# Kernel tuning notes

Hardware: AMD Instinct MI355X
Metric: run time of the kernel (lower is better)

Reference implementation:

```python
import jax, jax.numpy as jnp
import numpy as np

B, S, D = 16, 2048, 2048  # S == D required for m_q + output broadcast in original code


def setup_inputs() -> dict:
    key = jax.random.key(0)
    ks = jax.random.split(key, 8)
    scale = 1.0 / np.sqrt(D)
    return {
        "hidden_list": jax.random.normal(ks[0], (B, S, D), dtype=jnp.float32),
        "m_q": jax.random.normal(ks[1], (D,), dtype=jnp.float32),
        "Wq": jax.random.normal(ks[2], (D, D), dtype=jnp.float32) * scale,
        "bq": jax.random.normal(ks[3], (D,), dtype=jnp.float32) * scale,
        "Wm": jax.random.normal(ks[4], (D, D), dtype=jnp.float32) * scale,
        "bm": jax.random.normal(ks[5], (D,), dtype=jnp.float32) * scale,
        "Wa": jax.random.normal(ks[6], (D, D), dtype=jnp.float32) * scale,
        "ba": jax.random.normal(ks[7], (D,), dtype=jnp.float32) * scale,
    }


def reference(hidden_list, m_q, Wq, bq, Wm, bm, Wa, ba):
    # hidden_list: [B, S, D]; m_q: [D]
    hq = jnp.tanh(jnp.einsum("bsd,ed->bse", hidden_list, Wq) + bq)      # [B,S,D]
    mq = jnp.tanh(Wm @ m_q + bm)                                        # [D]
    Sg = hq * mq                                                        # gated bilinear, [B,S,D]
    alpha = jax.nn.softmax(jnp.einsum("bsd,ed->bse", Sg, Wa) + ba, axis=-1)  # [B,S,D]
    output = jnp.sum(alpha * hidden_list, axis=-1)                      # [B,S]
    m_q_new = m_q + output                                              # broadcast [D]+[B,S] (S==D)
    return output, m_q_new
```

## Files before the change

### kernel.cpp

```cpp
#include <hip/hip_runtime.h>

typedef unsigned short u16;
typedef short bf16x8 __attribute__((ext_vector_type(8)));
typedef u16 u16x8 __attribute__((ext_vector_type(8)));
typedef float f32x4 __attribute__((ext_vector_type(4)));

__device__ __forceinline__ float bf2f(u16 u) {
    union { unsigned u; float f; } c; c.u = ((unsigned)u) << 16; return c.f;
}
__device__ __forceinline__ u16 f2bf(float f) {
    union { float f; unsigned u; } c; c.f = f;
    unsigned r = c.u + 0x7FFFu + ((c.u >> 16) & 1u);
    return (u16)(r >> 16);
}
__device__ __forceinline__ float tanh_fast(float x) {
    float e = __expf(2.0f * x);
    return 1.0f - 2.0f / (e + 1.0f);
}
__device__ __forceinline__ void gll16(const void* g, void* l) {
    __builtin_amdgcn_global_load_lds((const __attribute__((address_space(1))) void*)g,
                                     (__attribute__((address_space(3))) void*)l, 16, 0, 0);
}

#define BAR() do { __builtin_amdgcn_sched_barrier(0); __builtin_amdgcn_s_barrier(); \
                   __builtin_amdgcn_sched_barrier(0); } while (0)

__global__ __launch_bounds__(256) void cvt_f32_bf16(const float* __restrict__ src,
                                                    u16* __restrict__ dst, int n8) {
    int i = blockIdx.x * blockDim.x + threadIdx.x;
    int stride = gridDim.x * blockDim.x;
    for (; i < n8; i += stride) {
        const float4* s = (const float4*)(src + (size_t)i * 8);
        float4 a = s[0], b = s[1];
        u16x8 o;
        o[0] = f2bf(a.x); o[1] = f2bf(a.y); o[2] = f2bf(a.z); o[3] = f2bf(a.w);
        o[4] = f2bf(b.x); o[5] = f2bf(b.y); o[6] = f2bf(b.z); o[7] = f2bf(b.w);
        *(u16x8*)(dst + (size_t)i * 8) = o;
    }
}

__global__ __launch_bounds__(256) void mq_kernel(const float* __restrict__ Wm,
                                                 const float* __restrict__ q,
                                                 const float* __restrict__ bm,
                                                 float* __restrict__ mq, int D) {
    int w = threadIdx.x >> 6, l = threadIdx.x & 63;
    int e = blockIdx.x * 4 + w;
    const float* wp = Wm + (size_t)e * D;
    float s = 0.f;
    for (int j = 0; j < D; j += 256) {
        float4 wv = *(const float4*)(wp + j + l * 4);
        float4 qv = *(const float4*)(q + j + l * 4);
        s += wv.x * qv.x + wv.y * qv.y + wv.z * qv.z + wv.w * qv.w;
    }
    #pragma unroll
    for (int o = 32; o >= 1; o >>= 1) s += __shfl_xor(s, o);
    if (l == 0) mq[e] = tanh_fast(s + bm[e]);
}

template <int EPI>
__global__ __launch_bounds__(512, 2) void gemm8(const u16* __restrict__ A,
                                                const u16* __restrict__ B,
                                                const float* __restrict__ bias,
                                                const float* __restrict__ gate,
                                                u16* __restrict__ C,
                                                int M, int N, int K) {
    __shared__ u16 sh[65536];
    char* LDS = (char*)sh;
    const int K2 = K * 2;
    const int KT = K >> 6;

    const int tid = threadIdx.x;
    const int w = tid >> 6, l = tid & 63;
    const int wm = w >> 2, wn = w & 3;

    int orig = blockIdx.x + gridDim.x * blockIdx.y;
    int nwg = gridDim.x * gridDim.y;
    int id = ((nwg & 7) == 0) ? ((orig & 7) * (nwg >> 3) + (orig >> 3)) : orig;
    const int tileN = (id % gridDim.x) * 256;
    const int tileM = (id / gridDim.x) * 256;

    const int r0 = (w * 2) * 8 + (l >> 3);
    const int r1 = (w * 2 + 1) * 8 + (l >> 3);
    const int cc = ((l & 7) ^ (l >> 3)) << 4;
    const char* srcA0 = (const char*)A + (size_t)(tileM + r0) * K2 + cc;
    const char* srcA1 = (const char*)A + (size_t)(tileM + r1) * K2 + cc;
    const char* srcB0 = (const char*)B + (size_t)(tileN + r0) * K2 + cc;
    const char* srcB1 = (const char*)B + (size_t)(tileN + r1) * K2 + cc;
    const int ldc0 = (w * 2) * 1024, ldc1 = (w * 2 + 1) * 1024;

#define STG_A(tk, h) do { size_t go = (size_t)(tk) * 128 + (size_t)(h) * 128 * K2; \
    int sb = ((((tk) & 1) * 2 + (h)) * 16384); \
    gll16(srcA0 + go, LDS + sb + ldc0); gll16(srcA1 + go, LDS + sb + ldc1); } while (0)
#define STG_B(tk, h) do { size_t go = (size_t)(tk) * 128 + (size_t)(h) * 128 * K2; \
    int sb = 65536 + ((((tk) & 1) * 2 + (h)) * 16384); \
    gll16(srcB0 + go, LDS + sb + ldc0); gll16(srcB1 + go, LDS + sb + ldc1); } while (0)

    const int sw = l & 7;
    const int rowA = (wm * 64 + (l & 15)) * 128;
    const int rowB = (wn * 32 + (l & 15)) * 128;
    const int ck0 = (((l >> 4) ^ sw) << 4);
    const int ck1 = (((4 + (l >> 4)) ^ sw) << 4);
    const char* pA0 = LDS + rowA + ck0;
    const char* pA1 = LDS + rowA + ck1;
    const char* pB0 = LDS + 65536 + rowB + ck0;
    const char* pB1 = LDS + 65536 + rowB + ck1;

    f32x4 acc[2][4][2][2] = {};

    STG_A(0, 0); STG_A(0, 1); STG_B(0, 0); STG_B(0, 1);
    STG_A(1, 0); STG_B(1, 0);
    asm volatile("s_waitcnt vmcnt(4)" ::: "memory");
    BAR();

#define MFMA_CLUSTER(QM, QN, AF, BF)                                            \
    __builtin_amdgcn_s_setprio(1);                                              \
    _Pragma("unroll")                                                           \
    for (int fm = 0; fm < 4; ++fm)                                              \
        _Pragma("unroll")                                                       \
        for (int fn = 0; fn < 2; ++fn) {                                        \
            acc[QM][fm][QN][fn] = __builtin_amdgcn_mfma_f32_16x16x32_bf16(      \
                AF[fm][0], BF[fn][0], acc[QM][fm][QN][fn], 0, 0, 0);            \
            acc[QM][fm][QN][fn] = __builtin_amdgcn_mfma_f32_16x16x32_bf16(      \
                AF[fm][1], BF[fn][1], acc[QM][fm][QN][fn], 0, 0, 0);            \
        }                                                                       \
    __builtin_amdgcn_s_setprio(0);

#define ITER(t, P) do {                                                         \
    constexpr int A0O = (2 * (P)) * 16384;                                      \
    constexpr int A1O = (2 * (P) + 1) * 16384;                                  \
    bf16x8 af[4][2], b0[2][2], b1[2][2];                                        \
                                   \
    _Pragma("unroll")                                                           \
    for (int fm = 0; fm < 4; ++fm) {                                            \
        af[fm][0] = *(const bf16x8*)(pA0 + A0O + fm * 2048);                    \
        af[fm][1] = *(const bf16x8*)(pA1 + A0O + fm * 2048);                    \
    }                                                                           \
    _Pragma("unroll")                                                           \
    for (int fn = 0; fn < 2; ++fn) {                                            \
        b0[fn][0] = *(const bf16x8*)(pB0 + A0O + fn * 2048);                    \
        b0[fn][1] = *(const bf16x8*)(pB1 + A0O + fn * 2048);                    \
    }                                                                           \
    if ((t) + 1 < KT) STG_A((t) + 1, 1);                                        \
    BAR();                                                                      \
    MFMA_CLUSTER(0, 0, af, b0)                                                  \
    BAR();                                                                      \
                                       \
    _Pragma("unroll")                                                           \
    for (int fn = 0; fn < 2; ++fn) {                                            \
        b1[fn][0] = *(const bf16x8*)(pB0 + A1O + fn * 2048);                    \
        b1[fn][1] = *(const bf16x8*)(pB1 + A1O + fn * 2048);                    \
    }                                                                           \
    if ((t) + 1 < KT) STG_B((t) + 1, 1);                                        \
    BAR();                                                                      \
    MFMA_CLUSTER(0, 1, af, b1)                                                  \
    BAR();                                                                      \
                                       \
    _Pragma("unroll")                                                           \
    for (int fm = 0; fm < 4; ++fm) {                                            \
        af[fm][0] = *(const bf16x8*)(pA0 + A1O + fm * 2048);                    \
        af[fm][1] = *(const bf16x8*)(pA1 + A1O + fm * 2048);                    \
    }                                                                           \
    if ((t) + 2 < KT) STG_A((t) + 2, 0);                                        \
    BAR();                                                                      \
    MFMA_CLUSTER(1, 0, af, b0)                                                  \
    BAR();                                                                      \
                                     \
    if ((t) + 2 < KT) STG_B((t) + 2, 0);                                        \
    BAR();                                                                      \
    MFMA_CLUSTER(1, 1, af, b1)                                                  \
    if ((t) + 2 < KT) asm volatile("s_waitcnt vmcnt(4)" ::: "memory");          \
    else              asm volatile("s_waitcnt vmcnt(0)" ::: "memory");          \
    BAR();                                                                      \
} while (0)

    for (int tt = 0; tt < KT; tt += 2) {
        ITER(tt, 0);
        ITER(tt + 1, 1);
    }
#undef ITER
#undef MFMA_CLUSTER
#undef STG_A
#undef STG_B

    const int cr = (l >> 4) * 4;
    const int cl = l & 15;
    #pragma unroll
    for (int qn = 0; qn < 2; ++qn)
        #pragma unroll
        for (int fn = 0; fn < 2; ++fn) {
            const int col = tileN + qn * 128 + wn * 32 + fn * 16 + cl;
            const float bs = bias[col];
            float gt = 0.f;
            if (EPI == 0) gt = gate[col];
            #pragma unroll
            for (int qm = 0; qm < 2; ++qm)
                #pragma unroll
                for (int fm = 0; fm < 4; ++fm)
                    #pragma unroll
                    for (int r = 0; r < 4; ++r) {
                        const int row = tileM + qm * 128 + wm * 64 + fm * 16 + cr + r;
                        float v = acc[qm][fm][qn][fn][r] + bs;
                        if (EPI == 0) v = tanh_fast(v) * gt;
                        C[(size_t)row * N + col] = f2bf(v);
                    }
        }
}

__global__ __launch_bounds__(256) void softmax_out(const u16* __restrict__ logits,
                                                   const float* __restrict__ hidden,
                                                   const float* __restrict__ m_q,
                                                   float* __restrict__ out,
                                                   int D, int R) {
    const int r = blockIdx.x;
    const int t = threadIdx.x;
    const int w = t >> 6, l = t & 63;
    const u16* lp = logits + (size_t)r * D + t * 8;
    const float* hp = hidden + (size_t)r * D + t * 8;

    bf16x8 lv = *(const bf16x8*)lp;
    float lf[8];
    #pragma unroll
    for (int j = 0; j < 8; ++j) lf[j] = bf2f((u16)lv[j]);
    float4 h0 = *(const float4*)hp;
    float4 h1 = *(const float4*)(hp + 4);
    float hv[8] = {h0.x, h0.y, h0.z, h0.w, h1.x, h1.y, h1.z, h1.w};

    float m = lf[0];
    #pragma unroll
    for (int j = 1; j < 8; ++j) m = fmaxf(m, lf[j]);
    #pragma unroll
    for (int o = 32; o >= 1; o >>= 1) m = fmaxf(m, __shfl_xor(m, o));

    __shared__ float red[8];
    if (l == 0) red[w] = m;
    __syncthreads();
    m = fmaxf(fmaxf(red[0], red[1]), fmaxf(red[2], red[3]));
    __syncthreads();

    float se = 0.f, sh = 0.f;
    #pragma unroll
    for (int j = 0; j < 8; ++j) {
        float e = __expf(lf[j] - m);
        se += e;
        sh += e * hv[j];
    }
    #pragma unroll
    for (int o = 32; o >= 1; o >>= 1) { se += __shfl_xor(se, o); sh += __shfl_xor(sh, o); }
    if (l == 0) { red[w] = se; red[4 + w] = sh; }
    __syncthreads();
    if (t == 0) {
        float SE = red[0] + red[1] + red[2] + red[3];
        float SH = red[4] + red[5] + red[6] + red[7];
        float o = SH / SE;
        out[r] = o;
        out[R + r] = m_q[r & (D - 1)] + o;
    }
}

extern "C" void kernel_launch(void* const* d_in, const int* in_sizes, int n_in,
                              void* d_out, int out_size, void* d_ws, size_t ws_size,
                              hipStream_t stream) {
    const float* hidden = (const float*)d_in[0];
    const float* m_q    = (const float*)d_in[1];
    const float* Wq     = (const float*)d_in[2];
    const float* bq     = (const float*)d_in[3];
    const float* Wm     = (const float*)d_in[4];
    const float* bm     = (const float*)d_in[5];
    const float* Wa     = (const float*)d_in[6];
    const float* ba     = (const float*)d_in[7];
    float* out = (float*)d_out;

    const int D = 2048;
    const int M = 16 * 2048;

    char* ws = (char*)d_ws;
    size_t oH  = 0;
    size_t oS  = oH  + (size_t)M * D * 2;
    size_t oWq = oS  + (size_t)M * D * 2;
    size_t oWa = oWq + (size_t)D * D * 2;
    size_t oMq = oWa + (size_t)D * D * 2;
    size_t need = oMq + (size_t)D * sizeof(float);
    if (ws_size < need) return;

    u16* hbf    = (u16*)(ws + oH);
    u16* Sg     = (u16*)(ws + oS);
    u16* Wqb    = (u16*)(ws + oWq);
    u16* Wab    = (u16*)(ws + oWa);
    float* mq   = (float*)(ws + oMq);
    u16* logits = hbf;

    cvt_f32_bf16<<<4096, 256, 0, stream>>>(hidden, hbf, M * D / 8);
    cvt_f32_bf16<<<1024, 256, 0, stream>>>(Wq, Wqb, D * D / 8);
    cvt_f32_bf16<<<1024, 256, 0, stream>>>(Wa, Wab, D * D / 8);
    mq_kernel<<<D / 4, 256, 0, stream>>>(Wm, m_q, bm, mq, D);

    dim3 grid(D / 256, M / 256);
    gemm8<0><<<grid, 512, 0, stream>>>(hbf, Wqb, bq, mq, Sg, M, D, D);
    gemm8<1><<<grid, 512, 0, stream>>>(Sg, Wab, ba, nullptr, logits, M, D, D);

    softmax_out<<<M, 256, 0, stream>>>(logits, hidden, m_q, out, D, M);
}
```

Baseline: 659.7 us.

## Software-pipeline LDS fragment loads with MFMA clusters and cut barriers

Restructures the GEMM main loop so the LDS fragment reads for the next quadrant are issued before or alongside the current MFMA cluster, using double-buffered A and B register fragments. The next tile's first-half fragments are prefetched at the end of each iteration. Barriers drop from seven to four per iteration and the vmcnt waits move. This is meant to hide LDS latency behind MFMA work and reduce sync stalls, at the cost of higher register pressure and a more delicate wait and barrier ordering.

```diff
diff --git a/kernel.cpp b/kernel.cpp
--- a/kernel.cpp
+++ b/kernel.cpp
@@ -106,11 +106,22 @@
     const char* pB1 = LDS + 65536 + rowB + ck1;
 
     f32x4 acc[2][4][2][2] = {};
-
-    STG_A(0, 0); STG_A(0, 1); STG_B(0, 0); STG_B(0, 1);
+    bf16x8 afA[4][2], afB[4][2], bb0[2][2], bb1[2][2];
+
+    STG_A(0, 0); STG_B(0, 0); STG_A(0, 1); STG_B(0, 1);
     STG_A(1, 0); STG_B(1, 0);
     asm volatile("s_waitcnt vmcnt(4)" ::: "memory");
     BAR();
+    #pragma unroll
+    for (int fm = 0; fm < 4; ++fm) {
+        afA[fm][0] = *(const bf16x8*)(pA0 + fm * 2048);
+        afA[fm][1] = *(const bf16x8*)(pA1 + fm * 2048);
+    }
+    #pragma unroll
+    for (int fn = 0; fn < 2; ++fn) {
+        bb0[fn][0] = *(const bf16x8*)(pB0 + fn * 2048);
+        bb0[fn][1] = *(const bf16x8*)(pB1 + fn * 2048);
+    }
 
 #define MFMA_CLUSTER(QM, QN, AF, BF)                                            \
     __builtin_amdgcn_s_setprio(1);                                              \
@@ -126,50 +137,51 @@
     __builtin_amdgcn_s_setprio(0);
 
 #define ITER(t, P) do {                                                         \
-    constexpr int A0O = (2 * (P)) * 16384;                                      \
-    constexpr int A1O = (2 * (P) + 1) * 16384;                                  \
-    bf16x8 af[4][2], b0[2][2], b1[2][2];                                        \
-                                   \
+    constexpr int S1 = (2 * (P) + 1) * 16384;                                   \
+    constexpr int SN = (2 * (1 - (P))) * 16384;                                 \
+              \
+    if ((t) + 1 < KT) STG_A((t) + 1, 1);                                        \
+    _Pragma("unroll")                                                           \
+    for (int fn = 0; fn < 2; ++fn) {                                            \
+        bb1[fn][0] = *(const bf16x8*)(pB0 + S1 + fn * 2048);                    \
+        bb1[fn][1] = *(const bf16x8*)(pB1 + S1 + fn * 2048);                    \
+    }                                                                           \
+    MFMA_CLUSTER(0, 0, afA, bb0)                                                \
+    BAR();                                                                      \
+              \
+    if ((t) + 1 < KT) STG_B((t) + 1, 1);                                        \
     _Pragma("unroll")                                                           \
     for (int fm = 0; fm < 4; ++fm) {                                            \
-        af[fm][0] = *(const bf16x8*)(pA0 + A0O + fm * 2048);                    \
-        af[fm][1] = *(const bf16x8*)(pA1 + A0O + fm * 2048);                    \
+        afB[fm][0] = *(const bf16x8*)(pA0 + S1 + fm * 2048);                    \
+        afB[fm][1] = *(const bf16x8*)(pA1 + S1 + fm * 2048);                    \
     }                                                                           \
-    _Pragma("unroll")                                                           \
-    for (int fn = 0; fn < 2; ++fn) {                                            \
-        b0[fn][0] = *(const bf16x8*)(pB0 + A0O + fn * 2048);                    \
-        b0[fn][1] = *(const bf16x8*)(pB1 + A0O + fn * 2048);                    \
+    MFMA_CLUSTER(0, 1, afA, bb1)                                                \
+    BAR();                                                                      \
+              \
+    if ((t) + 2 < KT) { STG_A((t) + 2, 0);                                      \
+        asm volatile("s_waitcnt vmcnt(6)" ::: "memory"); }                      \
+    else if ((t) + 1 < KT)                                                      \
+        asm volatile("s_waitcnt vmcnt(4)" ::: "memory");                        \
+    MFMA_CLUSTER(1, 0, afB, bb0)                                                \
+    BAR();                                                                      \
+                                          \
+    if ((t) + 2 < KT) { STG_B((t) + 2, 0);                                      \
+        asm volatile("s_waitcnt vmcnt(4)" ::: "memory"); }                      \
+    else if ((t) + 1 < KT)                                                      \
+        asm volatile("s_waitcnt vmcnt(0)" ::: "memory");                        \
+    if ((t) + 1 < KT) {                                                         \
+        _Pragma("unroll")                                                       \
+        for (int fm = 0; fm < 4; ++fm) {                                        \
+            afA[fm][0] = *(const bf16x8*)(pA0 + SN + fm * 2048);                \
+            afA[fm][1] = *(const bf16x8*)(pA1 + SN + fm * 2048);                \
+        }                                                                       \
+        _Pragma("unroll")                                                       \
+        for (int fn = 0; fn < 2; ++fn) {                                        \
+            bb0[fn][0] = *(const bf16x8*)(pB0 + SN + fn * 2048);                \
+            bb0[fn][1] = *(const bf16x8*)(pB1 + SN + fn * 2048);                \
+        }                                                                       \
     }                                                                           \
-    if ((t) + 1 < KT) STG_A((t) + 1, 1);                                        \
-    BAR();                                                                      \
-    MFMA_CLUSTER(0, 0, af, b0)                                                  \
-    BAR();                                                                      \
-                                       \
-    _Pragma("unroll")                                                           \
-    for (int fn = 0; fn < 2; ++fn) {                                            \
-        b1[fn][0] = *(const bf16x8*)(pB0 + A1O + fn * 2048);                    \
-        b1[fn][1] = *(const bf16x8*)(pB1 + A1O + fn * 2048);                    \
-    }                                                                           \
-    if ((t) + 1 < KT) STG_B((t) + 1, 1);                                        \
-    BAR();                                                                      \
-    MFMA_CLUSTER(0, 1, af, b1)                                                  \
-    BAR();                                                                      \
-                                       \
-    _Pragma("unroll")                                                           \
-    for (int fm = 0; fm < 4; ++fm) {                                            \
-        af[fm][0] = *(const bf16x8*)(pA0 + A1O + fm * 2048);                    \
-        af[fm][1] = *(const bf16x8*)(pA1 + A1O + fm * 2048);                    \
-    }                                                                           \
-    if ((t) + 2 < KT) STG_A((t) + 2, 0);                                        \
-    BAR();                                                                      \
-    MFMA_CLUSTER(1, 0, af, b0)                                                  \
-    BAR();                                                                      \
-                                     \
-    if ((t) + 2 < KT) STG_B((t) + 2, 0);                                        \
-    BAR();                                                                      \
-    MFMA_CLUSTER(1, 1, af, b1)                                                  \
-    if ((t) + 2 < KT) asm volatile("s_waitcnt vmcnt(4)" ::: "memory");          \
-    else              asm volatile("s_waitcnt vmcnt(0)" ::: "memory");          \
+    MFMA_CLUSTER(1, 1, afB, bb1)                                                \
     BAR();                                                                      \
 } while (0)
 
```

Measured after the change: 655.5 us. Within noise of the previous version (-0.6%).

## Shrink GEMM tiles to 128x128 with 256 threads and simpler double buffering

Applied to the files above, without the earlier changes.

The bf16 MFMA GEMM goes from a 256x256 tile with 8 waves and a finely interleaved four-phase pipeline to a 128x128 tile with 4 waves, each computing a 64x64 sub-tile. Each iteration now does one LDS fragment load phase, issues the global-to-LDS prefetch two K-steps ahead, and runs a single MFMA cluster. LDS per block is halved. The aim is higher occupancy and more blocks to balance across CUs, at the cost of lower arithmetic intensity per byte loaded and more global traffic for the two large GEMMs.

```diff
diff --git a/kernel.cpp b/kernel.cpp
--- a/kernel.cpp
+++ b/kernel.cpp
@@ -58,118 +58,89 @@
 }
 
 template <int EPI>
-__global__ __launch_bounds__(512, 2) void gemm8(const u16* __restrict__ A,
+__global__ __launch_bounds__(256, 2) void gemm8(const u16* __restrict__ A,
                                                 const u16* __restrict__ B,
                                                 const float* __restrict__ bias,
                                                 const float* __restrict__ gate,
                                                 u16* __restrict__ C,
                                                 int M, int N, int K) {
-    __shared__ u16 sh[65536];
+    __shared__ u16 sh[32768];
     char* LDS = (char*)sh;
     const int K2 = K * 2;
     const int KT = K >> 6;
 
     const int tid = threadIdx.x;
     const int w = tid >> 6, l = tid & 63;
-    const int wm = w >> 2, wn = w & 3;
+    const int wm = w >> 1, wn = w & 1;
 
     int orig = blockIdx.x + gridDim.x * blockIdx.y;
     int nwg = gridDim.x * gridDim.y;
     int id = ((nwg & 7) == 0) ? ((orig & 7) * (nwg >> 3) + (orig >> 3)) : orig;
-    const int tileN = (id % gridDim.x) * 256;
-    const int tileM = (id / gridDim.x) * 256;
-
-    const int r0 = (w * 2) * 8 + (l >> 3);
-    const int r1 = (w * 2 + 1) * 8 + (l >> 3);
-    const int cc = ((l & 7) ^ (l >> 3)) << 4;
-    const char* srcA0 = (const char*)A + (size_t)(tileM + r0) * K2 + cc;
-    const char* srcA1 = (const char*)A + (size_t)(tileM + r1) * K2 + cc;
-    const char* srcB0 = (const char*)B + (size_t)(tileN + r0) * K2 + cc;
-    const char* srcB1 = (const char*)B + (size_t)(tileN + r1) * K2 + cc;
-    const int ldc0 = (w * 2) * 1024, ldc1 = (w * 2 + 1) * 1024;
-
-#define STG_A(tk, h) do { size_t go = (size_t)(tk) * 128 + (size_t)(h) * 128 * K2; \
-    int sb = ((((tk) & 1) * 2 + (h)) * 16384); \
-    gll16(srcA0 + go, LDS + sb + ldc0); gll16(srcA1 + go, LDS + sb + ldc1); } while (0)
-#define STG_B(tk, h) do { size_t go = (size_t)(tk) * 128 + (size_t)(h) * 128 * K2; \
-    int sb = 65536 + ((((tk) & 1) * 2 + (h)) * 16384); \
-    gll16(srcB0 + go, LDS + sb + ldc0); gll16(srcB1 + go, LDS + sb + ldc1); } while (0)
+    const int tileN = (id % gridDim.x) * 128;
+    const int tileM = (id / gridDim.x) * 128;
+
+    const int srow = tid >> 3;
+    const int cc = ((tid & 7) ^ (srow & 7)) << 4;
+    const char* srcA = (const char*)A + (size_t)(tileM + srow) * K2 + cc;
+    const char* srcB = (const char*)B + (size_t)(tileN + srow) * K2 + cc;
+    char* dstBase = LDS + tid * 16;
+    const size_t rowStep = (size_t)32 * K2;
+
+#define STG_A(tk) do { size_t go = (size_t)(tk) * 128; char* d = dstBase + (((tk) & 1) << 14); \
+    gll16(srcA + go,               d);         gll16(srcA + go + rowStep,     d + 4096);       \
+    gll16(srcA + go + 2 * rowStep, d + 8192);  gll16(srcA + go + 3 * rowStep, d + 12288); } while (0)
+#define STG_B(tk) do { size_t go = (size_t)(tk) * 128; char* d = dstBase + 32768 + (((tk) & 1) << 14); \
+    gll16(srcB + go,               d);         gll16(srcB + go + rowStep,     d + 4096);       \
+    gll16(srcB + go + 2 * rowStep, d + 8192);  gll16(srcB + go + 3 * rowStep, d + 12288); } while (0)
 
     const int sw = l & 7;
     const int rowA = (wm * 64 + (l & 15)) * 128;
-    const int rowB = (wn * 32 + (l & 15)) * 128;
+    const int rowB = (wn * 64 + (l & 15)) * 128;
     const int ck0 = (((l >> 4) ^ sw) << 4);
     const int ck1 = (((4 + (l >> 4)) ^ sw) << 4);
     const char* pA0 = LDS + rowA + ck0;
     const char* pA1 = LDS + rowA + ck1;
-    const char* pB0 = LDS + 65536 + rowB + ck0;
-    const char* pB1 = LDS + 65536 + rowB + ck1;
-
-    f32x4 acc[2][4][2][2] = {};
-
-    STG_A(0, 0); STG_A(0, 1); STG_B(0, 0); STG_B(0, 1);
-    STG_A(1, 0); STG_B(1, 0);
-    asm volatile("s_waitcnt vmcnt(4)" ::: "memory");
+    const char* pB0 = LDS + 32768 + rowB + ck0;
+    const char* pB1 = LDS + 32768 + rowB + ck1;
+
+    f32x4 acc[4][4] = {};
+
+    STG_A(0); STG_B(0); STG_A(1); STG_B(1);
+    asm volatile("s_waitcnt vmcnt(8)" ::: "memory");
     BAR();
 
-#define MFMA_CLUSTER(QM, QN, AF, BF)                                            \
+#define ITER(t, P) do {                                                         \
+    constexpr int SA = (P) * 16384;                                             \
+    bf16x8 af[4][2], bf[4][2];                                                  \
+               \
+    _Pragma("unroll")                                                           \
+    for (int fm = 0; fm < 4; ++fm) {                                            \
+        af[fm][0] = *(const bf16x8*)(pA0 + SA + fm * 2048);                     \
+        af[fm][1] = *(const bf16x8*)(pA1 + SA + fm * 2048);                     \
+    }                                                                           \
+    _Pragma("unroll")                                                           \
+    for (int fn = 0; fn < 4; ++fn) {                                            \
+        bf[fn][0] = *(const bf16x8*)(pB0 + SA + fn * 2048);                     \
+        bf[fn][1] = *(const bf16x8*)(pB1 + SA + fn * 2048);                     \
+    }                                                                           \
+    asm volatile("s_waitcnt lgkmcnt(0)" ::: "memory");                          \
+    __builtin_amdgcn_sched_barrier(0);                                          \
+    BAR();                                                                      \
+                \
+    if ((t) + 2 < KT) { STG_A((t) + 2); STG_B((t) + 2); }                       \
     __builtin_amdgcn_s_setprio(1);                                              \
     _Pragma("unroll")                                                           \
     for (int fm = 0; fm < 4; ++fm)                                              \
         _Pragma("unroll")                                                       \
-        for (int fn = 0; fn < 2; ++fn) {                                        \
-            acc[QM][fm][QN][fn] = __builtin_amdgcn_mfma_f32_16x16x32_bf16(      \
-                AF[fm][0], BF[fn][0], acc[QM][fm][QN][fn], 0, 0, 0);            \
-            acc[QM][fm][QN][fn] = __builtin_amdgcn_mfma_f32_16x16x32_bf16(      \
-                AF[fm][1], BF[fn][1], acc[QM][fm][QN][fn], 0, 0, 0);            \
+        for (int fn = 0; fn < 4; ++fn) {                                        \
+            acc[fm][fn] = __builtin_amdgcn_mfma_f32_16x16x32_bf16(              \
+                af[fm][0], bf[fn][0], acc[fm][fn], 0, 0, 0);                    \
+            acc[fm][fn] = __builtin_amdgcn_mfma_f32_16x16x32_bf16(              \
+                af[fm][1], bf[fn][1], acc[fm][fn], 0, 0, 0);                    \
         }                                                                       \
-    __builtin_amdgcn_s_setprio(0);
-
-#define ITER(t, P) do {                                                         \
-    constexpr int A0O = (2 * (P)) * 16384;                                      \
-    constexpr int A1O = (2 * (P) + 1) * 16384;                                  \
-    bf16x8 af[4][2], b0[2][2], b1[2][2];                                        \
-                                   \
-    _Pragma("unroll")                                                           \
-    for (int fm = 0; fm < 4; ++fm) {                                            \
-        af[fm][0] = *(const bf16x8*)(pA0 + A0O + fm * 2048);                    \
-        af[fm][1] = *(const bf16x8*)(pA1 + A0O + fm * 2048);                    \
-    }                                                                           \
-    _Pragma("unroll")                                                           \
-    for (int fn = 0; fn < 2; ++fn) {                                            \
-        b0[fn][0] = *(const bf16x8*)(pB0 + A0O + fn * 2048);                    \
-        b0[fn][1] = *(const bf16x8*)(pB1 + A0O + fn * 2048);                    \
-    }                                                                           \
-    if ((t) + 1 < KT) STG_A((t) + 1, 1);                                        \
-    BAR();                                                                      \
-    MFMA_CLUSTER(0, 0, af, b0)                                                  \
-    BAR();                                                                      \
-                                       \
-    _Pragma("unroll")                                                           \
-    for (int fn = 0; fn < 2; ++fn) {                                            \
-        b1[fn][0] = *(const bf16x8*)(pB0 + A1O + fn * 2048);                    \
-        b1[fn][1] = *(const bf16x8*)(pB1 + A1O + fn * 2048);                    \
-    }                                                                           \
-    if ((t) + 1 < KT) STG_B((t) + 1, 1);                                        \
-    BAR();                                                                      \
-    MFMA_CLUSTER(0, 1, af, b1)                                                  \
-    BAR();                                                                      \
-                                       \
-    _Pragma("unroll")                                                           \
-    for (int fm = 0; fm < 4; ++fm) {                                            \
-        af[fm][0] = *(const bf16x8*)(pA0 + A1O + fm * 2048);                    \
-        af[fm][1] = *(const bf16x8*)(pA1 + A1O + fm * 2048);                    \
-    }                                                                           \
-    if ((t) + 2 < KT) STG_A((t) + 2, 0);                                        \
-    BAR();                                                                      \
-    MFMA_CLUSTER(1, 0, af, b0)                                                  \
-    BAR();                                                                      \
-                                     \
-    if ((t) + 2 < KT) STG_B((t) + 2, 0);                                        \
-    BAR();                                                                      \
-    MFMA_CLUSTER(1, 1, af, b1)                                                  \
-    if ((t) + 2 < KT) asm volatile("s_waitcnt vmcnt(4)" ::: "memory");          \
-    else              asm volatile("s_waitcnt vmcnt(0)" ::: "memory");          \
+    __builtin_amdgcn_s_setprio(0);                                              \
+    if ((t) + 2 < KT)      asm volatile("s_waitcnt vmcnt(8)" ::: "memory");     \
+    else if ((t) + 1 < KT) asm volatile("s_waitcnt vmcnt(0)" ::: "memory");     \
     BAR();                                                                      \
 } while (0)
 
@@ -178,32 +149,27 @@
         ITER(tt + 1, 1);
     }
 #undef ITER
-#undef MFMA_CLUSTER
 #undef STG_A
 #undef STG_B
 
     const int cr = (l >> 4) * 4;
     const int cl = l & 15;
     #pragma unroll
-    for (int qn = 0; qn < 2; ++qn)
+    for (int fn = 0; fn < 4; ++fn) {
+        const int col = tileN + wn * 64 + fn * 16 + cl;
+        const float bs = bias[col];
+        float gt = 0.f;
+        if (EPI == 0) gt = gate[col];
         #pragma unroll
-        for (int fn = 0; fn < 2; ++fn) {
-            const int col = tileN + qn * 128 + wn * 32 + fn * 16 + cl;
-            const float bs = bias[col];
-            float gt = 0.f;
-            if (EPI == 0) gt = gate[col];
+        for (int fm = 0; fm < 4; ++fm)
             #pragma unroll
-            for (int qm = 0; qm < 2; ++qm)
-                #pragma unroll
-                for (int fm = 0; fm < 4; ++fm)
-                    #pragma unroll
-                    for (int r = 0; r < 4; ++r) {
-                        const int row = tileM + qm * 128 + wm * 64 + fm * 16 + cr + r;
-                        float v = acc[qm][fm][qn][fn][r] + bs;
-                        if (EPI == 0) v = tanh_fast(v) * gt;
-                        C[(size_t)row * N + col] = f2bf(v);
-                    }
-        }
+            for (int r = 0; r < 4; ++r) {
+                const int row = tileM + wm * 64 + fm * 16 + cr + r;
+                float v = acc[fm][fn][r] + bs;
+                if (EPI == 0) v = tanh_fast(v) * gt;
+                C[(size_t)row * N + col] = f2bf(v);
+            }
+    }
 }
 
 __global__ __launch_bounds__(256) void softmax_out(const u16* __restrict__ logits,
@@ -294,9 +260,9 @@
     cvt_f32_bf16<<<1024, 256, 0, stream>>>(Wa, Wab, D * D / 8);
     mq_kernel<<<D / 4, 256, 0, stream>>>(Wm, m_q, bm, mq, D);
 
-    dim3 grid(D / 256, M / 256);
-    gemm8<0><<<grid, 512, 0, stream>>>(hbf, Wqb, bq, mq, Sg, M, D, D);
-    gemm8<1><<<grid, 512, 0, stream>>>(Sg, Wab, ba, nullptr, logits, M, D, D);
+    dim3 grid(D / 128, M / 128);
+    gemm8<0><<<grid, 256, 0, stream>>>(hbf, Wqb, bq, mq, Sg, M, D, D);
+    gemm8<1><<<grid, 256, 0, stream>>>(Sg, Wab, ba, nullptr, logits, M, D, D);
 
     softmax_out<<<M, 256, 0, stream>>>(logits, hidden, m_q, out, D, M);
 }
```

Result: slower. 763.5 us (+15.7%).
